# Optimization experiments

Measured on AMD Instinct MI355X. Metric: run time of the kernel, lower is better.

Reference implementation:

```python
import jax, jax.numpy as jnp
import numpy as np

# J2 (von Mises) plane-strain elastoplasticity with linear isotropic hardening
# (faithful stand-in for pyprnn's J2Material: elastic predictor + radial return,
#  committed history = plastic strain tensor + accumulated plastic strain).
E_MOD = 3130.0   # Young's modulus (epoxy, MPa)
NU = 0.37        # Poisson ratio
SIG_Y = 64.8     # initial yield stress
H_ISO = 300.0    # linear isotropic hardening modulus
MU = E_MOD / (2.0 * (1.0 + NU))
LAM = E_MOD * NU / ((1.0 + NU) * (1.0 - 2.0 * NU))


def j2_update(eps, eps_p, alpha):
    """eps: [P,3] (exx, eyy, gamma_xy engineering); eps_p: [P,4] (xx,yy,zz,xy tensorial);
    alpha: [P] accumulated plastic strain. Returns (stress [P,3], eps_p_new, alpha_new)."""
    ee_xx = eps[:, 0] - eps_p[:, 0]
    ee_yy = eps[:, 1] - eps_p[:, 1]
    ee_zz = -eps_p[:, 2]                      # plane strain: total ezz = 0
    ee_xy = 0.5 * eps[:, 2] - eps_p[:, 3]     # tensorial shear
    tr = ee_xx + ee_yy + ee_zz
    # trial (elastic predictor) stress
    sxx = LAM * tr + 2.0 * MU * ee_xx
    syy = LAM * tr + 2.0 * MU * ee_yy
    szz = LAM * tr + 2.0 * MU * ee_zz
    sxy = 2.0 * MU * ee_xy
    p = (sxx + syy + szz) / 3.0
    dxx, dyy, dzz = sxx - p, syy - p, szz - p
    q = jnp.sqrt(1.5 * (dxx * dxx + dyy * dyy + dzz * dzz + 2.0 * sxy * sxy))
    f = q - (SIG_Y + H_ISO * alpha)
    dgam = jnp.maximum(f, 0.0) / (3.0 * MU + H_ISO)   # radial return, closed form
    qs = jnp.maximum(q, 1e-12)
    nxx, nyy, nzz, nxy = 1.5 * dxx / qs, 1.5 * dyy / qs, 1.5 * dzz / qs, 1.5 * sxy / qs
    two_mu_dg = 2.0 * MU * dgam
    sig = jnp.stack([sxx - two_mu_dg * nxx, syy - two_mu_dg * nyy, sxy - two_mu_dg * nxy], axis=-1)
    eps_p_new = eps_p + dgam[:, None] * jnp.stack([nxx, nyy, nzz, nxy], axis=-1)
    alpha_new = alpha + dgam
    return sig, eps_p_new, alpha_new


def setup_inputs() -> dict:
    key = jax.random.key(0)
    k1, k2, k3 = jax.random.split(key, 3)
    B, T, F = 16384, 128, 3
    MATPTS = 16
    L, O = MATPTS * F, 3
    x = jax.random.normal(k1, (B, T, F), dtype=jnp.float32) * 0.02  # strain paths
    W1 = jax.random.normal(k2, (L, F), dtype=jnp.float32) * (1.0 / np.sqrt(F))
    W2 = jax.random.normal(k3, (O, L), dtype=jnp.float32) * (1.0 / np.sqrt(L))
    return {"x": x, "W1": W1, "W2": W2}


def reference(x, W1, W2):
    B, T, F = x.shape
    L = W1.shape[0]
    P = B * (L // F)                 # total material points = batch * mat_pts
    W2s = jax.nn.softplus(W2)        # SoftLayer: positive weights, no bias
    xt = jnp.swapaxes(x, 0, 1)       # [T, B, F]

    def step(carry, xi):
        eps_p, alpha = carry
        lat = xi @ W1.T                       # fc1 (no bias): [B, L]
        eps = lat.reshape(P, F)               # per-material-point strain
        sig, eps_p, alpha = j2_update(eps, eps_p, alpha)   # update + commit
        out = sig.reshape(B, L) @ W2s.T       # fc2 softplus-weighted linear
        return (eps_p, alpha), out

    carry0 = (jnp.zeros((P, 4), jnp.float32), jnp.zeros((P,), jnp.float32))
    _, ys = jax.lax.scan(step, carry0, xt)    # ys: [T, B, O]
    return jnp.swapaxes(ys, 0, 1)             # [B, T, O]
```

## Files before the change

### kernel.cpp

```cpp
#include <hip/hip_runtime.h>
#include <math.h>


#define BLOCK 256
#define BPB 32
#define TSTEPS 128
#define ROWF (TSTEPS * 3)
#define ROWP 388

typedef float v2 __attribute__((ext_vector_type(2)));

static __device__ __forceinline__ v2 vfma(v2 a, v2 b, v2 c) {
    return __builtin_elementwise_fma(a, b, c);
}
static __device__ __forceinline__ v2 vmax(v2 a, v2 b) {
    return __builtin_elementwise_max(a, b);
}

#define DPP_ADDST(v, ctrl)                                                   \
    v += __int_as_float(__builtin_amdgcn_update_dpp(                         \
        0, __float_as_int(v), (ctrl), 0xf, 0xf, true))

#define RED8(v)                                                              \
    do { DPP_ADDST(v, 0xB1); DPP_ADDST(v, 0x4E); DPP_ADDST(v, 0x141); } while (0)

__global__ __launch_bounds__(BLOCK, 2)
void prnn_j2_kernel(const float* __restrict__ x,
                    const float* __restrict__ W1,
                    const float* __restrict__ W2,
                    float* __restrict__ out)
{
    constexpr float MU    = (float)(3130.0 / (2.0 * (1.0 + 0.37)));
    constexpr float LAM   = (float)(3130.0 * 0.37 / ((1.0 + 0.37) * (1.0 - 2.0 * 0.37)));
    constexpr float SIG_Y = 64.8f;
    constexpr float H_ISO = 300.0f;
    const float TWO_MU  = 2.0f * MU;
    const float INV_DEN = 1.0f / (3.0f * MU + H_ISO);
    const float K3P     = (3.0f * MU) * INV_DEN;
    const float HP      = H_ISO * INV_DEN;
    const float KBULK   = LAM + TWO_MU * (1.0f / 3.0f);
    const float C_Q2    = 6.0f * MU * MU;

    __shared__ float xs[BPB * ROWP + 12];

    const int tid = threadIdx.x;
    const int g   = tid >> 3;
    const int l   = tid & 7;
    const int blockBase = blockIdx.x * (BPB * ROWF);

    {
        const float4* xg = (const float4*)(x + blockBase);
        for (int i4 = tid; i4 < BPB * ROWF / 4; i4 += BLOCK) {
            int b  = i4 / (ROWF / 4);
            int r4 = i4 - b * (ROWF / 4);
            ((float4*)(xs + b * ROWP))[r4] = xg[i4];
        }
    }

    const int pa = l, pb = l + 8;
    v2 w1p[3][3], w2p[3][3];
    #pragma unroll
    for (int c = 0; c < 3; ++c)
        #pragma unroll
        for (int f = 0; f < 3; ++f) {
            w1p[c][f].x = W1[(3 * pa + c) * 3 + f];
            w1p[c][f].y = W1[(3 * pb + c) * 3 + f];
        }
    #pragma unroll
    for (int o = 0; o < 3; ++o)
        #pragma unroll
        for (int c = 0; c < 3; ++c) {
            float wa = W2[o * 48 + 3 * pa + c];
            float wb = W2[o * 48 + 3 * pb + c];
            w2p[o][c].x = fmaxf(wa, 0.0f) + log1pf(expf(-fabsf(wa)));
            w2p[o][c].y = fmaxf(wb, 0.0f) + log1pf(expf(-fabsf(wb)));
        }

    __syncthreads();

    v2 p0 = {0.f,0.f}, p1 = {0.f,0.f}, p2 = {0.f,0.f}, p3 = {0.f,0.f};
    v2 yld = {SIG_Y, SIG_Y};
    float* xrow = &xs[g * ROWP];
    const float4* xv = (const float4*)xrow;
    const bool wact = (l < 3);

#define J2_PHYS(x0_, x1_, x2_, o0_, o1_, o2_)                                \
  {                                                                          \
    const float x0s = (x0_), x1s = (x1_), x2s = (x2_);                       \
    const v2 x0 = {x0s, x0s}, x1 = {x1s, x1s}, x2 = {x2s, x2s};              \
    const v2 e0 = vfma(w1p[0][0], x0, vfma(w1p[0][1], x1, w1p[0][2] * x2));  \
    const v2 e1 = vfma(w1p[1][0], x0, vfma(w1p[1][1], x1, w1p[1][2] * x2));  \
    const v2 e2 = vfma(w1p[2][0], x0, vfma(w1p[2][1], x1, w1p[2][2] * x2));  \
    const v2 ee_xx = e0 - p0;                                                \
    const v2 ee_yy = e1 - p1;                                                \
    const v2 ee_xy = 0.5f * e2 - p3;                                         \
    const v2 tr = (ee_xx + ee_yy) - p2;                                      \
    const v2 c3 = tr * (1.0f / 3.0f);                                        \
    const v2 exd = ee_xx - c3;                                               \
    const v2 eyd = ee_yy - c3;                                               \
    const v2 ezd = -p2 - c3;                                                 \
    v2 u = exd * exd;                                                        \
    u = vfma(eyd, eyd, u);                                                   \
    u = vfma(ezd, ezd, u);                                                   \
    u = vfma(ee_xy * ee_xy, (v2){2.0f, 2.0f}, u);                            \
    const v2 q2 = vmax(C_Q2 * u, (v2){1e-24f, 1e-24f});                      \
    v2 rq;                                                                   \
    rq.x = __builtin_amdgcn_rsqf(q2.x);                                      \
    rq.y = __builtin_amdgcn_rsqf(q2.y);                                      \
    const v2 q = q2 * rq;                                                    \
    const v2 f = vmax(q - yld, (v2){0.0f, 0.0f});                            \
    yld = vfma((v2){HP, HP}, f, yld);                                        \
    const v2 k   = (K3P * f) * rq;                                           \
    const v2 omk = 1.0f - k;                                                 \
    const v2 pm  = KBULK * tr;                                               \
    const v2 s0 = vfma(TWO_MU * exd, omk, pm);                               \
    const v2 s1 = vfma(TWO_MU * eyd, omk, pm);                               \
    const v2 s2 = (TWO_MU * ee_xy) * omk;                                    \
    p0 = vfma(k, exd, p0);                                                   \
    p1 = vfma(k, eyd, p1);                                                   \
    p2 = vfma(k, ezd, p2);                                                   \
    p3 = vfma(k, ee_xy, p3);                                                 \
    v2 r0 = vfma(w2p[0][0], s0, vfma(w2p[0][1], s1, w2p[0][2] * s2));        \
    v2 r1 = vfma(w2p[1][0], s0, vfma(w2p[1][1], s1, w2p[1][2] * s2));        \
    v2 r2 = vfma(w2p[2][0], s0, vfma(w2p[2][1], s1, w2p[2][2] * s2));        \
    o0_ = r0.x + r0.y;                                                       \
    o1_ = r1.x + r1.y;                                                       \
    o2_ = r2.x + r2.y;                                                       \
  }

#define PHYS_BLOCK(r)                                                        \
    J2_PHYS(A0.x, A0.y, A0.z, r[0],  r[1],  r[2]);                           \
    J2_PHYS(A0.w, A1.x, A1.y, r[3],  r[4],  r[5]);                           \
    J2_PHYS(A1.z, A1.w, A2.x, r[6],  r[7],  r[8]);                           \
    J2_PHYS(A2.y, A2.z, A2.w, r[9],  r[10], r[11])

#define RED_WRITE(r, bi)                                                     \
  {                                                                          \
    _Pragma("unroll")                                                        \
    for (int i = 0; i < 12; ++i) { RED8(r[i]); }                             \
    if (wact) {                                                              \
        float* wp = xrow + 12 * (bi) + l;                                    \
        wp[0] = (l == 0) ? r[0] : ((l == 1) ? r[1]  : r[2]);                 \
        wp[3] = (l == 0) ? r[3] : ((l == 1) ? r[4]  : r[5]);                 \
        wp[6] = (l == 0) ? r[6] : ((l == 1) ? r[7]  : r[8]);                 \
        wp[9] = (l == 0) ? r[9] : ((l == 1) ? r[10] : r[11]);                \
    }                                                                        \
  }

    float4 A0 = xv[0], A1 = xv[1], A2 = xv[2];
    float rprev[12];

    {
        float4 An0 = xv[3], An1 = xv[4], An2 = xv[5];
        PHYS_BLOCK(rprev);
        A0 = An0; A1 = An1; A2 = An2;
    }

    for (int tb = 1; tb < TSTEPS / 4; ++tb) {
        float4 An0 = xv[3 * tb + 3];
        float4 An1 = xv[3 * tb + 4];
        float4 An2 = xv[3 * tb + 5];

        float rcur[12];
        PHYS_BLOCK(rcur);
        RED_WRITE(rprev, tb - 1);

        #pragma unroll
        for (int i = 0; i < 12; ++i) rprev[i] = rcur[i];
        A0 = An0; A1 = An1; A2 = An2;
    }

    RED_WRITE(rprev, TSTEPS / 4 - 1);

#undef PHYS_BLOCK
#undef RED_WRITE
#undef J2_PHYS

    __syncthreads();

    {
        float4* og = (float4*)(out + blockBase);
        for (int i4 = tid; i4 < BPB * ROWF / 4; i4 += BLOCK) {
            int b  = i4 / (ROWF / 4);
            int r4 = i4 - b * (ROWF / 4);
            og[i4] = ((const float4*)(xs + b * ROWP))[r4];
        }
    }
}

extern "C" void kernel_launch(void* const* d_in, const int* in_sizes, int n_in,
                              void* d_out, int out_size, void* d_ws, size_t ws_size,
                              hipStream_t stream) {
    const float* x  = (const float*)d_in[0];
    const float* W1 = (const float*)d_in[1];
    const float* W2 = (const float*)d_in[2];
    float* out = (float*)d_out;

    const int B = 16384;
    dim3 grid(B / BPB);
    dim3 block(BLOCK);
    prnn_j2_kernel<<<grid, block, 0, stream>>>(x, W1, W2, out);
}
```

Measured before the change: 122.9 us.

## Map one material point per lane with 16-lane groups and higher occupancy

Replaces the packed two-points-per-lane float2 computation with scalar code where each of 16 lanes handles one material point, halving rows per block and doubling the grid. The launch-bounds occupancy hint is raised from 2 to 4 blocks per CU, and the output reduction gains a fourth DPP stage across 16 lanes. This aims to hide the latency of the serial time recurrence with more waves, at the cost of losing packed FP32 math and adding reduction work.

```diff
diff --git a/kernel.cpp b/kernel.cpp
--- a/kernel.cpp
+++ b/kernel.cpp
@@ -3,28 +3,20 @@
 
 
 #define BLOCK 256
-#define BPB 32
+#define BPB 16
 #define TSTEPS 128
 #define ROWF (TSTEPS * 3)
 #define ROWP 388
-
-typedef float v2 __attribute__((ext_vector_type(2)));
-
-static __device__ __forceinline__ v2 vfma(v2 a, v2 b, v2 c) {
-    return __builtin_elementwise_fma(a, b, c);
-}
-static __device__ __forceinline__ v2 vmax(v2 a, v2 b) {
-    return __builtin_elementwise_max(a, b);
-}
 
 #define DPP_ADDST(v, ctrl)                                                   \
     v += __int_as_float(__builtin_amdgcn_update_dpp(                         \
         0, __float_as_int(v), (ctrl), 0xf, 0xf, true))
 
-#define RED8(v)                                                              \
-    do { DPP_ADDST(v, 0xB1); DPP_ADDST(v, 0x4E); DPP_ADDST(v, 0x141); } while (0)
+#define RED16(v)                                                             \
+    do { DPP_ADDST(v, 0xB1); DPP_ADDST(v, 0x4E);                             \
+         DPP_ADDST(v, 0x141); DPP_ADDST(v, 0x140); } while (0)
 
-__global__ __launch_bounds__(BLOCK, 2)
+__global__ __launch_bounds__(BLOCK, 4)
 void prnn_j2_kernel(const float* __restrict__ x,
                     const float* __restrict__ W1,
                     const float* __restrict__ W2,
@@ -44,8 +36,8 @@
     __shared__ float xs[BPB * ROWP + 12];
 
     const int tid = threadIdx.x;
-    const int g   = tid >> 3;
-    const int l   = tid & 7;
+    const int g   = tid >> 4;
+    const int m   = tid & 15;
     const int blockBase = blockIdx.x * (BPB * ROWF);
 
     {
@@ -57,75 +49,64 @@
         }
     }
 
-    const int pa = l, pb = l + 8;
-    v2 w1p[3][3], w2p[3][3];
+    float w1[3][3], w2s[3][3];
     #pragma unroll
     for (int c = 0; c < 3; ++c)
         #pragma unroll
-        for (int f = 0; f < 3; ++f) {
-            w1p[c][f].x = W1[(3 * pa + c) * 3 + f];
-            w1p[c][f].y = W1[(3 * pb + c) * 3 + f];
-        }
+        for (int f = 0; f < 3; ++f)
+            w1[c][f] = W1[(3 * m + c) * 3 + f];
     #pragma unroll
     for (int o = 0; o < 3; ++o)
         #pragma unroll
         for (int c = 0; c < 3; ++c) {
-            float wa = W2[o * 48 + 3 * pa + c];
-            float wb = W2[o * 48 + 3 * pb + c];
-            w2p[o][c].x = fmaxf(wa, 0.0f) + log1pf(expf(-fabsf(wa)));
-            w2p[o][c].y = fmaxf(wb, 0.0f) + log1pf(expf(-fabsf(wb)));
+            float w = W2[o * 48 + 3 * m + c];
+            w2s[o][c] = fmaxf(w, 0.0f) + log1pf(expf(-fabsf(w)));
         }
 
     __syncthreads();
 
-    v2 p0 = {0.f,0.f}, p1 = {0.f,0.f}, p2 = {0.f,0.f}, p3 = {0.f,0.f};
-    v2 yld = {SIG_Y, SIG_Y};
+    float p0 = 0.f, p1 = 0.f, p2 = 0.f, p3 = 0.f;
+    float yld = SIG_Y;
     float* xrow = &xs[g * ROWP];
     const float4* xv = (const float4*)xrow;
-    const bool wact = (l < 3);
+    const bool wact = (m < 3);
 
 #define J2_PHYS(x0_, x1_, x2_, o0_, o1_, o2_)                                \
   {                                                                          \
-    const float x0s = (x0_), x1s = (x1_), x2s = (x2_);                       \
-    const v2 x0 = {x0s, x0s}, x1 = {x1s, x1s}, x2 = {x2s, x2s};              \
-    const v2 e0 = vfma(w1p[0][0], x0, vfma(w1p[0][1], x1, w1p[0][2] * x2));  \
-    const v2 e1 = vfma(w1p[1][0], x0, vfma(w1p[1][1], x1, w1p[1][2] * x2));  \
-    const v2 e2 = vfma(w1p[2][0], x0, vfma(w1p[2][1], x1, w1p[2][2] * x2));  \
-    const v2 ee_xx = e0 - p0;                                                \
-    const v2 ee_yy = e1 - p1;                                                \
-    const v2 ee_xy = 0.5f * e2 - p3;                                         \
-    const v2 tr = (ee_xx + ee_yy) - p2;                                      \
-    const v2 c3 = tr * (1.0f / 3.0f);                                        \
-    const v2 exd = ee_xx - c3;                                               \
-    const v2 eyd = ee_yy - c3;                                               \
-    const v2 ezd = -p2 - c3;                                                 \
-    v2 u = exd * exd;                                                        \
-    u = vfma(eyd, eyd, u);                                                   \
-    u = vfma(ezd, ezd, u);                                                   \
-    u = vfma(ee_xy * ee_xy, (v2){2.0f, 2.0f}, u);                            \
-    const v2 q2 = vmax(C_Q2 * u, (v2){1e-24f, 1e-24f});                      \
-    v2 rq;                                                                   \
-    rq.x = __builtin_amdgcn_rsqf(q2.x);                                      \
-    rq.y = __builtin_amdgcn_rsqf(q2.y);                                      \
-    const v2 q = q2 * rq;                                                    \
-    const v2 f = vmax(q - yld, (v2){0.0f, 0.0f});                            \
-    yld = vfma((v2){HP, HP}, f, yld);                                        \
-    const v2 k   = (K3P * f) * rq;                                           \
-    const v2 omk = 1.0f - k;                                                 \
-    const v2 pm  = KBULK * tr;                                               \
-    const v2 s0 = vfma(TWO_MU * exd, omk, pm);                               \
-    const v2 s1 = vfma(TWO_MU * eyd, omk, pm);                               \
-    const v2 s2 = (TWO_MU * ee_xy) * omk;                                    \
-    p0 = vfma(k, exd, p0);                                                   \
-    p1 = vfma(k, eyd, p1);                                                   \
-    p2 = vfma(k, ezd, p2);                                                   \
-    p3 = vfma(k, ee_xy, p3);                                                 \
-    v2 r0 = vfma(w2p[0][0], s0, vfma(w2p[0][1], s1, w2p[0][2] * s2));        \
-    v2 r1 = vfma(w2p[1][0], s0, vfma(w2p[1][1], s1, w2p[1][2] * s2));        \
-    v2 r2 = vfma(w2p[2][0], s0, vfma(w2p[2][1], s1, w2p[2][2] * s2));        \
-    o0_ = r0.x + r0.y;                                                       \
-    o1_ = r1.x + r1.y;                                                       \
-    o2_ = r2.x + r2.y;                                                       \
+    const float x0 = (x0_), x1 = (x1_), x2 = (x2_);                          \
+    const float e0 = w1[0][0]*x0 + w1[0][1]*x1 + w1[0][2]*x2;                \
+    const float e1 = w1[1][0]*x0 + w1[1][1]*x1 + w1[1][2]*x2;                \
+    const float e2 = w1[2][0]*x0 + w1[2][1]*x1 + w1[2][2]*x2;                \
+    const float ee_xx = e0 - p0;                                             \
+    const float ee_yy = e1 - p1;                                             \
+    const float ee_xy = fmaf(0.5f, e2, -p3);                                 \
+    const float tr = (ee_xx + ee_yy) - p2;                                   \
+    const float c3 = tr * (1.0f / 3.0f);                                     \
+    const float exd = ee_xx - c3;                                            \
+    const float eyd = ee_yy - c3;                                            \
+    const float ezd = -p2 - c3;                                              \
+    float u = exd * exd;                                                     \
+    u = fmaf(eyd, eyd, u);                                                   \
+    u = fmaf(ezd, ezd, u);                                                   \
+    u = fmaf(ee_xy * ee_xy, 2.0f, u);                                        \
+    const float q2 = fmaxf(C_Q2 * u, 1e-24f);                                \
+    const float rq = __builtin_amdgcn_rsqf(q2);                              \
+    const float q  = q2 * rq;                                                \
+    const float f  = fmaxf(q - yld, 0.0f);                                   \
+    yld = fmaf(HP, f, yld);                                                  \
+    const float k   = (K3P * f) * rq;                                        \
+    const float omk = 1.0f - k;                                              \
+    const float pm  = KBULK * tr;                                            \
+    const float s0 = fmaf(TWO_MU * exd, omk, pm);                            \
+    const float s1 = fmaf(TWO_MU * eyd, omk, pm);                            \
+    const float s2 = (TWO_MU * ee_xy) * omk;                                 \
+    p0 = fmaf(k, exd, p0);                                                   \
+    p1 = fmaf(k, eyd, p1);                                                   \
+    p2 = fmaf(k, ezd, p2);                                                   \
+    p3 = fmaf(k, ee_xy, p3);                                                 \
+    o0_ = w2s[0][0]*s0 + w2s[0][1]*s1 + w2s[0][2]*s2;                        \
+    o1_ = w2s[1][0]*s0 + w2s[1][1]*s1 + w2s[1][2]*s2;                        \
+    o2_ = w2s[2][0]*s0 + w2s[2][1]*s1 + w2s[2][2]*s2;                        \
   }
 
 #define PHYS_BLOCK(r)                                                        \
@@ -137,13 +118,13 @@
 #define RED_WRITE(r, bi)                                                     \
   {                                                                          \
     _Pragma("unroll")                                                        \
-    for (int i = 0; i < 12; ++i) { RED8(r[i]); }                             \
+    for (int i = 0; i < 12; ++i) { RED16(r[i]); }                            \
     if (wact) {                                                              \
-        float* wp = xrow + 12 * (bi) + l;                                    \
-        wp[0] = (l == 0) ? r[0] : ((l == 1) ? r[1]  : r[2]);                 \
-        wp[3] = (l == 0) ? r[3] : ((l == 1) ? r[4]  : r[5]);                 \
-        wp[6] = (l == 0) ? r[6] : ((l == 1) ? r[7]  : r[8]);                 \
-        wp[9] = (l == 0) ? r[9] : ((l == 1) ? r[10] : r[11]);                \
+        float* wp = xrow + 12 * (bi) + m;                                    \
+        wp[0] = (m == 0) ? r[0] : ((m == 1) ? r[1]  : r[2]);                 \
+        wp[3] = (m == 0) ? r[3] : ((m == 1) ? r[4]  : r[5]);                 \
+        wp[6] = (m == 0) ? r[6] : ((m == 1) ? r[7]  : r[8]);                 \
+        wp[9] = (m == 0) ? r[9] : ((m == 1) ? r[10] : r[11]);                \
     }                                                                        \
   }
 
```

New measurement: 136.6 us. +11.2%, slower.
